# Kernel optimization log

Hardware: AMD Instinct MI355X
Metric: run time of the kernel (lower is better)

The kernel has to match this reference:

```python
import jax, jax.numpy as jnp
import numpy as np

N_CLASSES = 100
EPSILON = 1e-07


def setup_inputs() -> dict:
    key = jax.random.key(0)
    k1, k2 = jax.random.split(key)
    y_pred = jax.random.normal(k1, (2000000, N_CLASSES), dtype=jnp.float32)
    y_true = jax.random.randint(k2, (2000000,), 0, N_CLASSES, dtype=jnp.int64)
    return {"y_pred": y_pred, "y_true": y_true}


def reference(y_pred, y_true):
    C = N_CLASSES
    pred = jnp.argmax(y_pred, axis=1)  # [N]
    # confusion matrix: rows = true class, cols = predicted class
    flat_idx = y_true.astype(jnp.int32) * C + pred.astype(jnp.int32)
    conf = jnp.zeros((C * C,), dtype=y_pred.dtype).at[flat_idx].add(1.0).reshape(C, C)
    TP = jnp.diag(conf)                      # [C]
    col_sum = jnp.sum(conf, axis=0)          # [C] sum over rows for each predicted label
    FN = col_sum - TP                        # original: conf[idx!=label, label].sum()
    sensitivity = jnp.sum(TP / (TP + FN + EPSILON)) / C
    return sensitivity
```

## Files before the change

### kernel.cpp

```cpp
#include <hip/hip_runtime.h>
#include <stdint.h>

#define N_CLASSES 100
#define ROWS_PER_TILE 64
#define BLOCK 320
#define F4_PER_TILE 1600
#define LOADS_PER_THREAD 5
#define EPS 1e-7f

__device__ __forceinline__ void lds_dma16(void* lds, const void* g) {
    __builtin_amdgcn_global_load_lds(
        (const __attribute__((address_space(1))) uint32_t*)g,
        (__attribute__((address_space(3))) uint32_t*)lds, 16, 0, 0);
}

__global__ __launch_bounds__(BLOCK) void sens_count_kernel(
    const float* __restrict__ y_pred, const int* __restrict__ y_true,
    unsigned int* __restrict__ counters, int n_rows)
{
    __shared__ float s_rows[2][ROWS_PER_TILE * N_CLASSES];
    __shared__ unsigned int s_pc[N_CLASSES];
    __shared__ unsigned int s_tp[N_CLASSES];

    const int tid = threadIdx.x;
    for (int i = tid; i < N_CLASSES; i += BLOCK) { s_pc[i] = 0u; s_tp[i] = 0u; }
    __syncthreads();

    const long long n_tiles = ((long long)n_rows + ROWS_PER_TILE - 1) / ROWS_PER_TILE;
    const long long total_f4 = (long long)n_rows * (N_CLASSES / 4);

    auto issue_tile = [&](long long t, int b) {
        const long long base_f4 = t * (long long)F4_PER_TILE;
        float* dst = s_rows[b];
        #pragma unroll
        for (int k = 0; k < LOADS_PER_THREAD; ++k) {
            const int i = k * BLOCK + tid;
            long long gi = base_f4 + i;
            if (gi >= total_f4) gi = total_f4 - 1;
            lds_dma16(dst + (size_t)i * 4, y_pred + gi * 4);
        }
    };

    long long tile = blockIdx.x;
    int cur = 0;
    if (tile < n_tiles) issue_tile(tile, 0);

    for (; tile < n_tiles; tile += gridDim.x) {
        const int r = tid >> 2;
        const int q = tid & 3;
        const long long grow = tile * ROWS_PER_TILE + r;

        int tv = -1;
        if (tid < 256 && grow < n_rows) tv = y_true[grow];

        const long long next = tile + gridDim.x;
        if (next < n_tiles) {
            issue_tile(next, cur ^ 1);
            asm volatile("s_waitcnt vmcnt(5)" ::: "memory");
        } else {
            asm volatile("s_waitcnt vmcnt(0)" ::: "memory");
        }
        asm volatile("s_barrier" ::: "memory");

        if (tid < 256 && grow < n_rows) {
            const float* rowp = &s_rows[cur][r * N_CLASSES + q * 25];
            float best = rowp[0];
            int bidx = q * 25;
            #pragma unroll
            for (int t2 = 1; t2 < 25; ++t2) {
                float v = rowp[t2];
                if (v > best) { best = v; bidx = q * 25 + t2; }
            }
            #pragma unroll
            for (int m = 1; m <= 2; m <<= 1) {
                float ov = __shfl_xor(best, m, 64);
                int   oi = __shfl_xor(bidx, m, 64);
                if (ov > best || (ov == best && oi < bidx)) { best = ov; bidx = oi; }
            }
            if (q == 0) {
                atomicAdd(&s_pc[bidx], 1u);
                if (tv == bidx) atomicAdd(&s_tp[bidx], 1u);
            }
        }
        asm volatile("s_barrier" ::: "memory");
        cur ^= 1;
    }

    __syncthreads();
    for (int i = tid; i < N_CLASSES; i += BLOCK) {
        unsigned int pc = s_pc[i], tp = s_tp[i];
        if (pc) atomicAdd(&counters[i], pc);
        if (tp) atomicAdd(&counters[N_CLASSES + i], tp);
    }
}

__global__ void sens_final_kernel(const unsigned int* __restrict__ counters,
                                  float* __restrict__ out)
{
    const int lane = threadIdx.x;
    float acc = 0.f;
    for (int c = lane; c < N_CLASSES; c += 64) {
        float pc = (float)counters[c];
        float tp = (float)counters[N_CLASSES + c];
        acc += tp / (pc + EPS);
    }
    #pragma unroll
    for (int m = 32; m >= 1; m >>= 1) acc += __shfl_xor(acc, m, 64);
    if (lane == 0) out[0] = acc / (float)N_CLASSES;
}

extern "C" void kernel_launch(void* const* d_in, const int* in_sizes, int n_in,
                              void* d_out, int out_size, void* d_ws, size_t ws_size,
                              hipStream_t stream)
{
    const float* y_pred = (const float*)d_in[0];
    const int*   y_true = (const int*)d_in[1];
    float* out = (float*)d_out;
    const int n_rows = in_sizes[1];

    unsigned int* counters = (unsigned int*)d_ws;
    hipMemsetAsync(counters, 0, 2 * N_CLASSES * sizeof(unsigned int), stream);

    long long n_tiles = ((long long)n_rows + ROWS_PER_TILE - 1) / ROWS_PER_TILE;
    int grid = 768;
    if (n_tiles < grid) grid = (int)n_tiles;

    sens_count_kernel<<<grid, BLOCK, 0, stream>>>(y_pred, y_true, counters, n_rows);
    sens_final_kernel<<<1, 64, 0, stream>>>(counters, out);
}
```

Measured before the change: 165.5 us.

## Give each wave private double-buffered LDS tiles and drop block barriers

Restructures the streaming argmax so each wave loads and processes its own 16-row tile with its own double buffer, removing the two block-wide barriers per iteration. Loads switch from 16-byte to 4-byte LDS DMA so 64 lanes cover a 1600-dword tile contiguously, with a fast path for full tiles. This aims to remove inter-wave stalls but increases the number of memory instructions per byte.

```diff
diff --git a/kernel.cpp b/kernel.cpp
--- a/kernel.cpp
+++ b/kernel.cpp
@@ -2,74 +2,87 @@
 #include <stdint.h>
 
 #define N_CLASSES 100
-#define ROWS_PER_TILE 64
-#define BLOCK 320
-#define F4_PER_TILE 1600
-#define LOADS_PER_THREAD 5
+#define ROWS_PER_WTILE 16
+#define DW_PER_WTILE (ROWS_PER_WTILE * N_CLASSES)
+#define LOADS_PER_LANE (DW_PER_WTILE / 64)
+#define BLOCK 256
+#define WAVES_PER_BLOCK (BLOCK / 64)
 #define EPS 1e-7f
 
-__device__ __forceinline__ void lds_dma16(void* lds, const void* g) {
+__device__ __forceinline__ void lds_dma4(void* lds, const void* g) {
     __builtin_amdgcn_global_load_lds(
         (const __attribute__((address_space(1))) uint32_t*)g,
-        (__attribute__((address_space(3))) uint32_t*)lds, 16, 0, 0);
+        (__attribute__((address_space(3))) uint32_t*)lds, 4, 0, 0);
 }
 
 __global__ __launch_bounds__(BLOCK) void sens_count_kernel(
     const float* __restrict__ y_pred, const int* __restrict__ y_true,
     unsigned int* __restrict__ counters, int n_rows)
 {
-    __shared__ float s_rows[2][ROWS_PER_TILE * N_CLASSES];
+    __shared__ float s_rows[WAVES_PER_BLOCK][2][DW_PER_WTILE];
     __shared__ unsigned int s_pc[N_CLASSES];
     __shared__ unsigned int s_tp[N_CLASSES];
 
-    const int tid = threadIdx.x;
+    const int tid  = threadIdx.x;
+    const int wave = tid >> 6;
+    const int lane = tid & 63;
+
     for (int i = tid; i < N_CLASSES; i += BLOCK) { s_pc[i] = 0u; s_tp[i] = 0u; }
     __syncthreads();
 
-    const long long n_tiles = ((long long)n_rows + ROWS_PER_TILE - 1) / ROWS_PER_TILE;
-    const long long total_f4 = (long long)n_rows * (N_CLASSES / 4);
+    const long long n_wtiles = ((long long)n_rows + ROWS_PER_WTILE - 1) / ROWS_PER_WTILE;
+    const long long total_dw = (long long)n_rows * N_CLASSES;
+    const long long stride   = (long long)gridDim.x * WAVES_PER_BLOCK;
 
-    auto issue_tile = [&](long long t, int b) {
-        const long long base_f4 = t * (long long)F4_PER_TILE;
-        float* dst = s_rows[b];
-        #pragma unroll
-        for (int k = 0; k < LOADS_PER_THREAD; ++k) {
-            const int i = k * BLOCK + tid;
-            long long gi = base_f4 + i;
-            if (gi >= total_f4) gi = total_f4 - 1;
-            lds_dma16(dst + (size_t)i * 4, y_pred + gi * 4);
+    auto issue = [&](long long t, int b) {
+        const long long base = t * (long long)DW_PER_WTILE;
+        float* dst = s_rows[wave][b];
+        const float* gp = y_pred + base;
+        if (base + DW_PER_WTILE <= total_dw) {
+            #pragma unroll
+            for (int k = 0; k < LOADS_PER_LANE; ++k) {
+                const int i = k * 64 + lane;
+                lds_dma4(dst + i, gp + i);
+            }
+        } else {
+            #pragma unroll
+            for (int k = 0; k < LOADS_PER_LANE; ++k) {
+                const int i = k * 64 + lane;
+                long long gi = base + i;
+                if (gi >= total_dw) gi = total_dw - 1;
+                lds_dma4(dst + i, y_pred + gi);
+            }
         }
     };
 
-    long long tile = blockIdx.x;
+    long long t = (long long)blockIdx.x * WAVES_PER_BLOCK + wave;
     int cur = 0;
-    if (tile < n_tiles) issue_tile(tile, 0);
+    if (t < n_wtiles) issue(t, 0);
 
-    for (; tile < n_tiles; tile += gridDim.x) {
-        const int r = tid >> 2;
-        const int q = tid & 3;
-        const long long grow = tile * ROWS_PER_TILE + r;
+    for (; t < n_wtiles; t += stride) {
+        const int r = lane >> 2;
+        const int q = lane & 3;
+        const long long grow = t * ROWS_PER_WTILE + r;
 
         int tv = -1;
-        if (tid < 256 && grow < n_rows) tv = y_true[grow];
+        if (grow < (long long)n_rows) tv = y_true[grow];
 
-        const long long next = tile + gridDim.x;
-        if (next < n_tiles) {
-            issue_tile(next, cur ^ 1);
-            asm volatile("s_waitcnt vmcnt(5)" ::: "memory");
+        const long long nxt = t + stride;
+        if (nxt < n_wtiles) {
+            issue(nxt, cur ^ 1);
+            asm volatile("s_waitcnt vmcnt(25)" ::: "memory");
         } else {
             asm volatile("s_waitcnt vmcnt(0)" ::: "memory");
         }
-        asm volatile("s_barrier" ::: "memory");
 
-        if (tid < 256 && grow < n_rows) {
-            const float* rowp = &s_rows[cur][r * N_CLASSES + q * 25];
+        if (grow < (long long)n_rows) {
+            const float* rowp = &s_rows[wave][cur][r * N_CLASSES + q * 25];
             float best = rowp[0];
             int bidx = q * 25;
             #pragma unroll
-            for (int t2 = 1; t2 < 25; ++t2) {
-                float v = rowp[t2];
-                if (v > best) { best = v; bidx = q * 25 + t2; }
+            for (int i2 = 1; i2 < 25; ++i2) {
+                float v = rowp[i2];
+                if (v > best) { best = v; bidx = q * 25 + i2; }
             }
             #pragma unroll
             for (int m = 1; m <= 2; m <<= 1) {
@@ -82,7 +95,6 @@
                 if (tv == bidx) atomicAdd(&s_tp[bidx], 1u);
             }
         }
-        asm volatile("s_barrier" ::: "memory");
         cur ^= 1;
     }
 
@@ -121,10 +133,7 @@
     unsigned int* counters = (unsigned int*)d_ws;
     hipMemsetAsync(counters, 0, 2 * N_CLASSES * sizeof(unsigned int), stream);
 
-    long long n_tiles = ((long long)n_rows + ROWS_PER_TILE - 1) / ROWS_PER_TILE;
-    int grid = 768;
-    if (n_tiles < grid) grid = (int)n_tiles;
-
+    const int grid = 768;
     sens_count_kernel<<<grid, BLOCK, 0, stream>>>(y_pred, y_true, counters, n_rows);
     sens_final_kernel<<<1, 64, 0, stream>>>(counters, out);
 }
```

After: 148.4 us, median of 2. 10.3% less time.
